# Performance work log

Measured on AMD Instinct MI355X. Metric: run time of the kernel, lower is better.

## Reference

```python
import jax, jax.numpy as jnp
import numpy as np
from jax import lax

D_MODEL = 512
D_STATE = 32
D_CONV = 4
D_INNER = 2 * D_MODEL
DT_RANK = (D_MODEL + 15) // 16  # 32
B_SZ, L = 8, 1024
EPS = 1e-12


def _mamba_params(key, pfx):
    ks = jax.random.split(key, 6)
    s = 0.02
    p = {}
    p[pfx + '_in_w'] = jax.random.normal(ks[0], (2 * D_INNER, D_MODEL)) * s
    p[pfx + '_conv_w'] = jax.random.normal(ks[1], (D_INNER, D_CONV)) * s
    p[pfx + '_conv_b'] = jnp.zeros((D_INNER,))
    p[pfx + '_xproj_w'] = jax.random.normal(ks[2], (DT_RANK + 2 * D_STATE, D_INNER)) * s
    p[pfx + '_dt_w'] = jax.random.normal(ks[3], (D_INNER, DT_RANK)) * s
    p[pfx + '_dt_b'] = jax.random.uniform(ks[4], (D_INNER,), minval=-4.0, maxval=-2.0)
    p[pfx + '_A_log'] = jnp.log(jnp.broadcast_to(jnp.arange(1, D_STATE + 1, dtype=jnp.float32), (D_INNER, D_STATE)))
    p[pfx + '_D'] = jnp.ones((D_INNER,))
    p[pfx + '_out_w'] = jax.random.normal(ks[5], (D_MODEL, D_INNER)) * s
    return p


def setup_inputs() -> dict:
    key = jax.random.key(0)
    ks = jax.random.split(key, 10)
    inp = {
        'hidden_states': jax.random.normal(ks[0], (B_SZ, L, D_MODEL)),
        'lengths': jax.random.randint(ks[1], (B_SZ,), 1, L + 1, dtype=jnp.int32),
    }
    inp.update(_mamba_params(ks[2], 'f'))
    inp.update(_mamba_params(ks[3], 'b'))
    s = 0.02
    inp['proj_w'] = jax.random.normal(ks[4], (1, 2)) * 0.5 + 0.5
    inp['proj_b'] = jnp.zeros((1,))
    inp['ln_g'] = jnp.ones((D_MODEL,))
    inp['ln_b'] = jnp.zeros((D_MODEL,))
    inp['ffn_w1'] = jax.random.normal(ks[5], (4 * D_MODEL, D_MODEL)) * s
    inp['ffn_b1'] = jnp.zeros((4 * D_MODEL,))
    inp['ffn_w2'] = jax.random.normal(ks[6], (D_MODEL, 4 * D_MODEL)) * s
    inp['ffn_b2'] = jnp.zeros((D_MODEL,))
    inp['ffn_ln_g'] = jnp.ones((D_MODEL,))
    inp['ffn_ln_b'] = jnp.zeros((D_MODEL,))
    return inp


def _layernorm(x, g, b):
    mu = jnp.mean(x, -1, keepdims=True)
    var = jnp.mean(jnp.square(x - mu), -1, keepdims=True)
    return (x - mu) * lax.rsqrt(var + EPS) * g + b


def _selective_scan(delta, Bm, Cm, u, A, D):
    # delta,u: (B,L,Di); Bm,Cm: (B,L,N); A: (Di,N); D: (Di,)
    def step(h, inp):
        d_t, B_t, C_t, u_t = inp
        dA = jnp.exp(d_t[..., None] * A)                 # (B,Di,N)
        h = dA * h + (d_t * u_t)[..., None] * B_t[:, None, :]
        y = jnp.einsum('bdn,bn->bd', h, C_t)
        return h, y
    h0 = jnp.zeros((u.shape[0], A.shape[0], A.shape[1]), u.dtype)
    xs = (delta.transpose(1, 0, 2), Bm.transpose(1, 0, 2),
          Cm.transpose(1, 0, 2), u.transpose(1, 0, 2))
    _, ys = lax.scan(step, h0, xs)
    return ys.transpose(1, 0, 2) + u * D


def _mamba(x, in_w, conv_w, conv_b, xproj_w, dt_w, dt_b, A_log, Dp, out_w):
    xz = jnp.einsum('bld,ed->ble', x, in_w)              # (B,L,2Di)
    x_in, z = jnp.split(xz, 2, axis=-1)
    # causal depthwise conv1d
    xc = jnp.pad(x_in.transpose(0, 2, 1), ((0, 0), (0, 0), (D_CONV - 1, 0)))
    xc = lax.conv_general_dilated(xc, conv_w[:, None, :], (1,), 'VALID',
                                  dimension_numbers=('NCH', 'OIH', 'NCH'),
                                  feature_group_count=D_INNER)
    xc = jax.nn.silu(xc + conv_b[None, :, None]).transpose(0, 2, 1)  # (B,L,Di)
    x_dbl = jnp.einsum('bld,ed->ble', xc, xproj_w)
    dt, Bm, Cm = jnp.split(x_dbl, [DT_RANK, DT_RANK + D_STATE], axis=-1)
    delta = jax.nn.softplus(jnp.einsum('blr,dr->bld', dt, dt_w) + dt_b)
    A = -jnp.exp(A_log)
    y = _selective_scan(delta, Bm, Cm, xc, A, Dp)
    y = y * jax.nn.silu(z)
    return jnp.einsum('bld,ed->ble', y, out_w)


def reference(hidden_states, lengths,
              f_in_w, f_conv_w, f_conv_b, f_xproj_w, f_dt_w, f_dt_b, f_A_log, f_D, f_out_w,
              b_in_w, b_conv_w, b_conv_b, b_xproj_w, b_dt_w, b_dt_b, b_A_log, b_D, b_out_w,
              proj_w, proj_b, ln_g, ln_b,
              ffn_w1, ffn_b1, ffn_w2, ffn_b2, ffn_ln_g, ffn_ln_b):
    x = hidden_states
    hf = _mamba(x, f_in_w, f_conv_w, f_conv_b, f_xproj_w, f_dt_w, f_dt_b, f_A_log, f_D, f_out_w)
    hb = _mamba(jnp.flip(x, 1), b_in_w, b_conv_w, b_conv_b, b_xproj_w, b_dt_w, b_dt_b, b_A_log, b_D, b_out_w)
    hb = jnp.flip(hb, 1)
    # Linear(2,1) over stacked [hf,hb] on last axis
    out = hf * proj_w[0, 0] + hb * proj_w[0, 1] + proj_b[0]
    out1 = _layernorm(out + x, ln_g, ln_b)  # dropout = identity (eval)
    h = jax.nn.gelu(jnp.einsum('bld,ed->ble', out1, ffn_w1) + ffn_b1, approximate=False)
    h = jnp.einsum('ble,de->bld', h, ffn_w2) + ffn_b2
    return _layernorm(h + out1, ffn_ln_g, ffn_ln_b)
```

## Files before the change

### kernel.cpp

```cpp
#include <hip/hip_runtime.h>
#include <hip/hip_bf16.h>
#include <hip/hip_fp16.h>
#include <math.h>

typedef __hip_bfloat16 bf16;
typedef __attribute__((ext_vector_type(8))) short bfrag;
typedef __attribute__((ext_vector_type(4))) float ffrag;
typedef __attribute__((ext_vector_type(4))) float f4;
typedef __attribute__((ext_vector_type(4))) short sh4;

#define BSZ    8
#define LSEQ   1024
#define DMODEL 512
#define DINNER 1024
#define DSTATE 32
#define DTRANK 32
#define MROWS  (BSZ * LSEQ)

__device__ __forceinline__ float bf2f(bf16 v) { return __bfloat162float(v); }
__device__ __forceinline__ float s2f(short s) {
    union { unsigned u; float f; } c; c.u = ((unsigned)(unsigned short)s) << 16; return c.f;
}
__device__ __forceinline__ short f2s(float v) {
    union { bf16 b; short s; } u; u.b = __float2bfloat16(v); return u.s;
}
__device__ __forceinline__ void stC(float* p, size_t i, float v) { p[i] = v; }
__device__ __forceinline__ void stC(bf16* p, size_t i, float v) { p[i] = __float2bfloat16(v); }
__device__ __forceinline__ float fsigmoid(float x) {
    return __builtin_amdgcn_rcpf(1.f + __expf(-x));
}
__device__ __forceinline__ float fexp2(float x) { return __builtin_amdgcn_exp2f(x); }

__device__ __forceinline__ float dload(const void* p, size_t i, int f) {
    if (f == 1) return ((const float*)p)[i];
    if (f == 2) return __half2float(((const __half*)p)[i]);
    if (f == 3) return (float)((const double*)p)[i];
    return bf2f(((const bf16*)p)[i]);
}

enum { ACT_NONE = 0, ACT_SOFTPLUS = 1, ACT_GELU = 2 };

__global__ void resolve_kernel(const void* a8, const void* d9, const void* d22,
                               const void* s0, const void* s1, int* flags)
{
    if (threadIdx.x != 0 || blockIdx.x != 0) return;
    const int cand[4] = {1, 0, 2, 3};
    int fw = -1;
    for (int ci = 0; ci < 4 && fw < 0; ++ci) {
        int f = cand[ci];
        bool ok = true;
        for (int k = 0; k < 48 && ok; ++k) {
            float e = logf((float)((k & 31) + 1));
            float v = dload(a8, k, f);
            ok = (v == v) && fabsf(v - e) <= 0.02f * e + 0.02f;
        }
        for (int k = 0; k < 8 && ok; ++k)
            ok = fabsf(dload(d9, k, f) - 1.f) <= 0.01f &&
                 fabsf(dload(d22, k, f) - 1.f) <= 0.01f;
        if (ok) fw = f;
    }
    int fx = -1, xs = -1;
    for (int si = 0; si < 2 && fx < 0; ++si) {
        const void* p = (si == 0) ? s0 : s1;
        for (int ci = 0; ci < 4 && fx < 0; ++ci) {
            int f = cand[ci];
            bool ok = true;
            float s = 0.f, s2 = 0.f;
            for (int k = 0; k < 256 && ok; ++k) {
                float v = dload(p, k, f);
                ok = (v == v) && fabsf(v) < 16.f;
                s += v; s2 += v * v;
            }
            if (ok) {
                float mu = s * (1.f / 256.f);
                float var = s2 * (1.f / 256.f) - mu * mu;
                if (var > 0.25f && var < 4.f) { fx = f; xs = si; }
            }
        }
    }
    flags[0] = (fw < 0) ? 1 : fw;
    flags[1] = (fx < 0) ? 1 : fx;
    flags[2] = (xs < 0) ? 0 : xs;
    flags[3] = (fw == 1 && fx == 1) ? 1 : 0;
}

__global__ __launch_bounds__(256) void cvt_x_kernel(const void* x0, const void* x1,
                                                    bf16* __restrict__ dst,
                                                    const int* __restrict__ flags)
{
    const void* x = flags[2] ? x1 : x0;
    const int fx = flags[1];
    int i = blockIdx.x * 256 + threadIdx.x;
    if (fx == 1) {
        f4 v = ((const f4*)x)[i];
        sh4 o;
#pragma unroll
        for (int j = 0; j < 4; ++j) o[j] = f2s(v[j]);
        ((sh4*)dst)[i] = o;
    } else {
#pragma unroll
        for (int j = 0; j < 4; ++j)
            dst[(size_t)i * 4 + j] = __float2bfloat16(dload(x, (size_t)i * 4 + j, fx));
    }
}

__global__ __launch_bounds__(256) void cvt_w_kernel(const float* __restrict__ src,
                                                    bf16* __restrict__ dst, int n4)
{
    int i = blockIdx.x * 256 + threadIdx.x;
    if (i >= n4) return;
    f4 v = ((const f4*)src)[i];
    sh4 o;
#pragma unroll
    for (int j = 0; j < 4; ++j) o[j] = f2s(v[j]);
    ((sh4*)dst)[i] = o;
}

__device__ __forceinline__ void glds16(const bf16* g, short* l)
{
    __builtin_amdgcn_global_load_lds(
        (const __attribute__((address_space(1))) void*)g,
        (__attribute__((address_space(3))) void*)l,
        16, 0, 0);
}

template <int FLIPB, int ACT, typename CT>
__global__ __launch_bounds__(256) void bgemm_kernel(
    const bf16* __restrict__ A, int lda,
    const bf16* __restrict__ B, int ldb,
    const float* __restrict__ bias,
    CT* __restrict__ C, int ldc, int K)
{
    __shared__ __align__(16) short As[128 * 32];
    __shared__ __align__(16) short Bs[128 * 32];
    const int tid = threadIdx.x;
    const int bm = blockIdx.y * 128, bn = blockIdx.x * 128;
    const int lane = tid & 63, w = tid >> 6;

    const int srow = lane >> 2;
    const int skc  = (lane & 3) << 3;
    const int arow0 = bm + w * 32 + srow;
    int brow0 = bn + w * 32 + srow;
    int brow1 = brow0 + 16;
    if (FLIPB) {
        brow0 = (brow0 & ~(LSEQ - 1)) + (LSEQ - 1 - (brow0 & (LSEQ - 1)));
        brow1 = (brow1 & ~(LSEQ - 1)) + (LSEQ - 1 - (brow1 & (LSEQ - 1)));
    }
    const bf16* ga0 = A + (size_t)arow0 * lda + skc;
    const bf16* ga1 = ga0 + (size_t)16 * lda;
    const bf16* gb0 = B + (size_t)brow0 * ldb + skc;
    const bf16* gb1 = B + (size_t)brow1 * ldb + skc;
    short* la0 = &As[(w * 32) * 32];
    short* la1 = &As[(w * 32 + 16) * 32];
    short* lb0 = &Bs[(w * 32) * 32];
    short* lb1 = &Bs[(w * 32 + 16) * 32];

    const int wm = (w & 1) << 6, wn = (w >> 1) << 6;
    const int lm = lane & 15, quad = lane >> 4;

    ffrag acc[4][4];
#pragma unroll
    for (int i = 0; i < 4; ++i)
#pragma unroll
        for (int j = 0; j < 4; ++j)
#pragma unroll
            for (int e = 0; e < 4; ++e) acc[i][j][e] = 0.f;

    for (int k0 = 0; k0 < K; k0 += 32) {
        glds16(ga0 + k0, la0);
        glds16(ga1 + k0, la1);
        glds16(gb0 + k0, lb0);
        glds16(gb1 + k0, lb1);
        __syncthreads();
        bfrag af[4], bfv[4];
#pragma unroll
        for (int ti = 0; ti < 4; ++ti)
            af[ti] = *(const bfrag*)&As[(wm + ti * 16 + lm) * 32 + quad * 8];
#pragma unroll
        for (int tj = 0; tj < 4; ++tj)
            bfv[tj] = *(const bfrag*)&Bs[(wn + tj * 16 + lm) * 32 + quad * 8];
#pragma unroll
        for (int ti = 0; ti < 4; ++ti)
#pragma unroll
            for (int tj = 0; tj < 4; ++tj)
                acc[ti][tj] = __builtin_amdgcn_mfma_f32_16x16x32_bf16(
                    af[ti], bfv[tj], acc[ti][tj], 0, 0, 0);
        __syncthreads();
    }

#pragma unroll
    for (int tj = 0; tj < 4; ++tj) {
        int col = bn + wn + tj * 16 + lm;
        float bcv = bias ? bias[col] : 0.f;
#pragma unroll
        for (int ti = 0; ti < 4; ++ti) {
#pragma unroll
            for (int r2 = 0; r2 < 4; ++r2) {
                int rowg = bm + wm + ti * 16 + quad * 4 + r2;
                float v = acc[ti][tj][r2] + bcv;
                if (ACT == ACT_GELU) v = 0.5f * v * (1.f + erff(v * 0.70710678118654752f));
                stC(C, (size_t)rowg * ldc + col, v);
            }
        }
    }
}

template <int AM, int WHID, int FLIPW, int ACT, int BROW, typename CT>
__global__ __launch_bounds__(256) void mgemm_kernel(
    const void* __restrict__ A, int lda,
    const void* __restrict__ W0, const void* __restrict__ W1, int ldw,
    const float* __restrict__ bias,
    CT* __restrict__ C, int ldc, int M, int N, int K,
    const int* __restrict__ flags)
{
    __shared__ short As[128 * 40];
    __shared__ short Ws[128 * 40];
    const int tid = threadIdx.x;
    const int bm = blockIdx.y * 128;
    const int bn = blockIdx.x * 128;
    const float* Wp = (const float*)(WHID ? (flags[2] ? W1 : W0) : W0);

    const int r = tid >> 1;
    const int hcol = (tid & 1) << 4;
    int wrow = bn + r;
    if (FLIPW) { int b = wrow >> 10, l = wrow & 1023; wrow = (b << 10) + (1023 - l); }

    const int lane = tid & 63, w = tid >> 6;
    const int wm = (w & 1) << 6, wn = (w >> 1) << 6;
    const int lm = lane & 15, quad = lane >> 4;

    ffrag acc[4][4];
#pragma unroll
    for (int i = 0; i < 4; ++i)
#pragma unroll
        for (int j = 0; j < 4; ++j)
#pragma unroll
            for (int e = 0; e < 4; ++e) acc[i][j][e] = 0.f;

    for (int k0 = 0; k0 < K; k0 += 32) {
        if (AM == 2) {
            int kk = tid >> 3;
            int mc = tid & 7;
            const bf16* src = (const bf16*)A + (size_t)(k0 + kk) * lda + bm + mc * 16;
            bfrag v0 = *(const bfrag*)src;
            bfrag v1 = *(const bfrag*)(src + 8);
#pragma unroll
            for (int i = 0; i < 8; ++i) {
                As[(mc * 16 + i) * 40 + kk] = v0[i];
                As[(mc * 16 + 8 + i) * 40 + kk] = v1[i];
            }
        } else if (AM == 0) {
            const bf16* src = (const bf16*)A + (size_t)(bm + r) * lda + k0 + hcol;
            *(bfrag*)&As[r * 40 + hcol] = *(const bfrag*)src;
            *(bfrag*)&As[r * 40 + hcol + 8] = *(const bfrag*)(src + 8);
        } else {
            const float* src = (const float*)A + (size_t)(bm + r) * lda + k0 + hcol;
            float t[16];
            ((f4*)t)[0] = ((const f4*)src)[0];
            ((f4*)t)[1] = ((const f4*)src)[1];
            ((f4*)t)[2] = ((const f4*)src)[2];
            ((f4*)t)[3] = ((const f4*)src)[3];
            bfrag s0, s1;
#pragma unroll
            for (int i = 0; i < 8; ++i) { s0[i] = f2s(t[i]); s1[i] = f2s(t[8 + i]); }
            *(bfrag*)&As[r * 40 + hcol] = s0;
            *(bfrag*)&As[r * 40 + hcol + 8] = s1;
        }
        {
            bfrag s0, s1;
            if (bn + r < N) {
                const float* src = Wp + (size_t)wrow * ldw + k0 + hcol;
                float t[16];
                ((f4*)t)[0] = ((const f4*)src)[0];
                ((f4*)t)[1] = ((const f4*)src)[1];
                ((f4*)t)[2] = ((const f4*)src)[2];
                ((f4*)t)[3] = ((const f4*)src)[3];
#pragma unroll
                for (int i = 0; i < 8; ++i) { s0[i] = f2s(t[i]); s1[i] = f2s(t[8 + i]); }
            } else {
#pragma unroll
                for (int i = 0; i < 8; ++i) { s0[i] = 0; s1[i] = 0; }
            }
            *(bfrag*)&Ws[r * 40 + hcol] = s0;
            *(bfrag*)&Ws[r * 40 + hcol + 8] = s1;
        }
        __syncthreads();

        bfrag af[4], bfv[4];
#pragma unroll
        for (int ti = 0; ti < 4; ++ti)
            af[ti] = *(const bfrag*)&As[(wm + ti * 16 + lm) * 40 + quad * 8];
#pragma unroll
        for (int tj = 0; tj < 4; ++tj)
            bfv[tj] = *(const bfrag*)&Ws[(wn + tj * 16 + lm) * 40 + quad * 8];
#pragma unroll
        for (int ti = 0; ti < 4; ++ti)
#pragma unroll
            for (int tj = 0; tj < 4; ++tj)
                acc[ti][tj] = __builtin_amdgcn_mfma_f32_16x16x32_bf16(
                    af[ti], bfv[tj], acc[ti][tj], 0, 0, 0);
        __syncthreads();
    }

#pragma unroll
    for (int tj = 0; tj < 4; ++tj) {
        int col = bn + wn + tj * 16 + lm;
        if (col < N) {
            float bcv = (bias && !BROW) ? bias[col] : 0.f;
#pragma unroll
            for (int ti = 0; ti < 4; ++ti) {
#pragma unroll
                for (int r2 = 0; r2 < 4; ++r2) {
                    int rowg = bm + wm + ti * 16 + quad * 4 + r2;
                    float v = acc[ti][tj][r2] + bcv;
                    if (BROW && bias) v += bias[rowg];
                    if (ACT == ACT_SOFTPLUS) v = (v > 20.f) ? v : log1pf(expf(v));
                    else if (ACT == ACT_GELU) v = 0.5f * v * (1.f + erff(v * 0.70710678118654752f));
                    stC(C, (size_t)rowg * ldc + col, v);
                }
            }
        }
    }
}

__global__ __launch_bounds__(256) void conv_silu_kernel(
    const bf16* __restrict__ xin_T,
    const void* __restrict__ cw,
    const void* __restrict__ cb,
    bf16* __restrict__ u_T,
    const int* __restrict__ flags)
{
    const int fw = flags[0];
    int blk = blockIdx.x;
    int chunk = blk & 3;
    int db = blk >> 2;
    int b = db & 7;
    int d = db >> 3;
    int l = chunk * 256 + threadIdx.x;
    size_t base = (size_t)d * MROWS + b * LSEQ;
    float w0 = dload(cw, d * 4 + 0, fw), w1 = dload(cw, d * 4 + 1, fw);
    float w2 = dload(cw, d * 4 + 2, fw), w3 = dload(cw, d * 4 + 3, fw);
    float acc = dload(cb, d, fw);
    if (l >= 3) acc += bf2f(xin_T[base + l - 3]) * w0;
    if (l >= 2) acc += bf2f(xin_T[base + l - 2]) * w1;
    if (l >= 1) acc += bf2f(xin_T[base + l - 1]) * w2;
    acc += bf2f(xin_T[base + l]) * w3;
    u_T[base + l] = __float2bfloat16(acc * fsigmoid(acc));
}

#define SCH 8
struct ScanBuf { float dl[SCH], uv[SCH], Bv[SCH], Cv[SCH]; float zsc, usc; };
struct PV { float p[SCH]; float zsc, usc; };

__device__ __forceinline__ void scan_load(ScanBuf& s,
    const bf16* __restrict__ dT, const bf16* __restrict__ uT,
    const bf16* __restrict__ zT, const float* __restrict__ xdbl,
    size_t lb, size_t mb, int n)
{
    bfrag dv = *(const bfrag*)&dT[lb];
    bfrag uv = *(const bfrag*)&uT[lb];
#pragma unroll
    for (int j = 0; j < SCH; ++j) { s.dl[j] = s2f(dv[j]); s.uv[j] = s2f(uv[j]); }
    s.zsc = bf2f(zT[lb + (n & 7)]);
    s.usc = bf2f(uT[lb + (n & 7)]);
#pragma unroll
    for (int j = 0; j < SCH; ++j) {
        s.Bv[j] = xdbl[(mb + j) * 96 + 32 + n];
        s.Cv[j] = xdbl[(mb + j) * 96 + 64 + n];
    }
}

__device__ __forceinline__ void scan_steps(const ScanBuf& s, float& h, float Ad2, PV& o)
{
#pragma unroll
    for (int j = 0; j < SCH; ++j) {
        float dlv = s.dl[j];
        float e = fexp2(dlv * Ad2);
        h = e * h + dlv * s.uv[j] * s.Bv[j];
        o.p[j] = h * s.Cv[j];
    }
    o.zsc = s.zsc; o.usc = s.usc;
}

__device__ __forceinline__ void reduce_store(const PV& v, float Dd,
    bf16* __restrict__ yT, size_t lb, bool b0, bool b1, bool b2, bool wr)
{
    float q[4];
#pragma unroll
    for (int jj = 0; jj < 4; ++jj) {
        float keep = b0 ? v.p[2 * jj + 1] : v.p[2 * jj];
        float send = b0 ? v.p[2 * jj] : v.p[2 * jj + 1];
        q[jj] = keep + __shfl_xor(send, 1);
    }
    float r0 = (b1 ? q[1] : q[0]) + __shfl_xor(b1 ? q[0] : q[1], 2);
    float r1 = (b1 ? q[3] : q[2]) + __shfl_xor(b1 ? q[2] : q[3], 2);
    float t = (b2 ? r1 : r0) + __shfl_xor(b2 ? r0 : r1, 4);
    t += __shfl_xor(t, 8);
    t += __shfl_xor(t, 16);
    if (wr) {
        float y = t + v.usc * Dd;
        float g = v.zsc;
        y *= g * fsigmoid(g);
        yT[lb + (threadIdx.x & 7)] = __float2bfloat16(y);
    }
}

__global__ __launch_bounds__(256) void scan_kernel(
    const bf16* __restrict__ delta_T,
    bf16* __restrict__ u_T,
    const bf16* __restrict__ z_T,
    const float* __restrict__ xdbl,
    const void* __restrict__ A_log,
    const void* __restrict__ Dp,
    const int* __restrict__ flags)
{
    const int fw = flags[0];
    const int tid = threadIdx.x;
    const int n = tid & 31;
    const int dloc = tid >> 5;
    const int gd = blockIdx.x * 8 + dloc;
    const int b = gd >> 10;
    const int d = gd & (DINNER - 1);
    const bool b0 = n & 1, b1 = n & 2, b2 = n & 4;
    const bool wr = (n < 8);

    const float Ad2 = -__expf(dload(A_log, d * DSTATE + n, fw)) * 1.44269504088896341f;
    const float Dd = dload(Dp, d, fw);
    const size_t lbase = (size_t)d * MROWS + b * LSEQ;
    const size_t mbase = (size_t)b * LSEQ;
    float h = 0.f;

    ScanBuf bufA, bufB;
    PV pA, pB;
    scan_load(bufA, delta_T, u_T, z_T, xdbl, lbase, mbase, n);
    scan_load(bufB, delta_T, u_T, z_T, xdbl, lbase + SCH, mbase + SCH, n);
    scan_steps(bufA, h, Ad2, pA);
    for (int c = 1; c < 127; c += 2) {
        scan_load(bufA, delta_T, u_T, z_T, xdbl,
                  lbase + (size_t)(c + 1) * SCH, mbase + (size_t)(c + 1) * SCH, n);
        scan_steps(bufB, h, Ad2, pB);
        reduce_store(pA, Dd, u_T, lbase + (size_t)(c - 1) * SCH, b0, b1, b2, wr);
        scan_load(bufB, delta_T, u_T, z_T, xdbl,
                  lbase + (size_t)(c + 2) * SCH, mbase + (size_t)(c + 2) * SCH, n);
        scan_steps(bufA, h, Ad2, pA);
        reduce_store(pB, Dd, u_T, lbase + (size_t)c * SCH, b0, b1, b2, wr);
    }
    scan_steps(bufB, h, Ad2, pB);
    reduce_store(pA, Dd, u_T, lbase + (size_t)126 * SCH, b0, b1, b2, wr);
    reduce_store(pB, Dd, u_T, lbase + (size_t)127 * SCH, b0, b1, b2, wr);
}

__global__ __launch_bounds__(256) void combine_ln_kernel(
    const bf16* __restrict__ hf, const bf16* __restrict__ hb,
    const void* __restrict__ x0, const void* __restrict__ x1,
    const void* __restrict__ pw, const void* __restrict__ pb,
    const void* __restrict__ g, const void* __restrict__ be,
    bf16* __restrict__ out1,
    const int* __restrict__ flags)
{
    const int fw = flags[0];
    const int fx = flags[1];
    const void* x = flags[2] ? x1 : x0;
    int row = blockIdx.x;
    int b = row >> 10, l = row & (LSEQ - 1);
    int rrow = (b << 10) + (LSEQ - 1 - l);
    float pw0 = dload(pw, 0, fw), pw1 = dload(pw, 1, fw), pbv = dload(pb, 0, fw);
    __shared__ float red[2][4];
    float v[2], s = 0.f, s2 = 0.f;
#pragma unroll
    for (int i = 0; i < 2; ++i) {
        int c = threadIdx.x + i * 256;
        float val = bf2f(hf[(size_t)row * DMODEL + c]) * pw0
                  + bf2f(hb[(size_t)rrow * DMODEL + c]) * pw1
                  + pbv + dload(x, (size_t)row * DMODEL + c, fx);
        v[i] = val; s += val; s2 += val * val;
    }
    for (int m = 1; m < 64; m <<= 1) { s += __shfl_xor(s, m); s2 += __shfl_xor(s2, m); }
    int w = threadIdx.x >> 6;
    if ((threadIdx.x & 63) == 0) { red[0][w] = s; red[1][w] = s2; }
    __syncthreads();
    s = red[0][0] + red[0][1] + red[0][2] + red[0][3];
    s2 = red[1][0] + red[1][1] + red[1][2] + red[1][3];
    float mu = s * (1.f / DMODEL);
    float var = s2 * (1.f / DMODEL) - mu * mu;
    float r = rsqrtf(fmaxf(var, 0.f) + 1e-12f);
#pragma unroll
    for (int i = 0; i < 2; ++i) {
        int c = threadIdx.x + i * 256;
        float val = (v[i] - mu) * r * dload(g, c, fw) + dload(be, c, fw);
        out1[(size_t)row * DMODEL + c] = __float2bfloat16(val);
    }
}

__global__ __launch_bounds__(256) void final_ln_kernel(
    const float* __restrict__ out2, const bf16* __restrict__ out1,
    const void* __restrict__ g, const void* __restrict__ be,
    float* __restrict__ out,
    const int* __restrict__ flags)
{
    const int fw = flags[0];
    const int valid = flags[3];
    int row = blockIdx.x;
    __shared__ float red[2][4];
    float v[2], s = 0.f, s2 = 0.f;
#pragma unroll
    for (int i = 0; i < 2; ++i) {
        int c = threadIdx.x + i * 256;
        float val = out2[(size_t)row * DMODEL + c] + bf2f(out1[(size_t)row * DMODEL + c]);
        v[i] = val; s += val; s2 += val * val;
    }
    for (int m = 1; m < 64; m <<= 1) { s += __shfl_xor(s, m); s2 += __shfl_xor(s2, m); }
    int w = threadIdx.x >> 6;
    if ((threadIdx.x & 63) == 0) { red[0][w] = s; red[1][w] = s2; }
    __syncthreads();
    s = red[0][0] + red[0][1] + red[0][2] + red[0][3];
    s2 = red[1][0] + red[1][1] + red[1][2] + red[1][3];
    float mu = s * (1.f / DMODEL);
    float var = s2 * (1.f / DMODEL) - mu * mu;
    float r = rsqrtf(fmaxf(var, 0.f) + 1e-12f);
#pragma unroll
    for (int i = 0; i < 2; ++i) {
        int c = threadIdx.x + i * 256;
        float val = (v[i] - mu) * r * dload(g, c, fw) + dload(be, c, fw);
        out[(size_t)row * DMODEL + c] = valid ? val : 0.f;
    }
}

extern "C" void kernel_launch(void* const* d_in, const int* in_sizes, int n_in,
                              void* d_out, int out_size, void* d_ws, size_t ws_size,
                              hipStream_t stream)
{
    const void* x0 = d_in[0];
    const void* x1 = d_in[1];
    const void* proj_w   = d_in[20];
    const void* proj_b   = d_in[21];
    const void* ln_g     = d_in[22];
    const void* ln_b     = d_in[23];
    const float* ffn_w1  = (const float*)d_in[24];
    const float* ffn_b1  = (const float*)d_in[25];
    const float* ffn_w2  = (const float*)d_in[26];
    const float* ffn_b2  = (const float*)d_in[27];
    const void* ffn_ln_g = d_in[28];
    const void* ffn_ln_b = d_in[29];

    char* wsb = (char*)d_ws;
    char* ob  = (char*)d_out;
    bf16*  xin_T   = (bf16*)(wsb + 0);
    bf16*  uy_T    = (bf16*)(wsb + (16u << 20));
    bf16*  z_T     = (bf16*)(wsb + (32u << 20));
    bf16*  delta_T = (bf16*)(wsb + 0);
    float* xdbl    = (float*)(wsb + (48u << 20));
    bf16*  in_w_bf = (bf16*)(wsb + (51u << 20));
    bf16*  hf      = (bf16*)d_out;
    bf16*  hb      = (bf16*)d_out + (size_t)MROWS * DMODEL;
    bf16*  xbf     = (bf16*)(ob + (8u << 20));
    bf16*  w1bf    = (bf16*)(ob + 0);
    bf16*  w2bf    = (bf16*)(ob + (2u << 20));
    bf16*  out1    = (bf16*)(wsb + 0);
    bf16*  ffn_h   = (bf16*)(wsb + (8u << 20));
    float* out2    = (float*)(wsb + (40u << 20));
    int*   flags   = (int*)(wsb + (56u << 20));

    dim3 blk(256);

    resolve_kernel<<<dim3(1), dim3(64), 0, stream>>>(
        d_in[8], d_in[9], d_in[22], x0, x1, flags);
    cvt_x_kernel<<<dim3(4096), blk, 0, stream>>>(x0, x1, xbf, flags);

    for (int dir = 0; dir < 2; ++dir) {
        int pb0 = 2 + dir * 9;
        const float* in_w    = (const float*)d_in[pb0 + 0];
        const void*  conv_w  = d_in[pb0 + 1];
        const void*  conv_b  = d_in[pb0 + 2];
        const float* xproj_w = (const float*)d_in[pb0 + 3];
        const float* dt_w    = (const float*)d_in[pb0 + 4];
        const float* dt_b    = (const float*)d_in[pb0 + 5];
        const void*  A_log   = d_in[pb0 + 6];
        const void*  Dp      = d_in[pb0 + 7];
        const float* out_w   = (const float*)d_in[pb0 + 8];
        bf16* hout = (dir == 0) ? hf : hb;

        cvt_w_kernel<<<dim3(1024), blk, 0, stream>>>(in_w, in_w_bf, (2048 * 512) / 4);
        if (dir == 0) {
            bgemm_kernel<0, ACT_NONE, bf16><<<dim3(64, 8), blk, 0, stream>>>(
                in_w_bf + (size_t)DINNER * DMODEL, DMODEL, xbf, DMODEL, nullptr,
                z_T, MROWS, DMODEL);
            bgemm_kernel<0, ACT_NONE, bf16><<<dim3(64, 8), blk, 0, stream>>>(
                in_w_bf, DMODEL, xbf, DMODEL, nullptr,
                xin_T, MROWS, DMODEL);
        } else {
            bgemm_kernel<1, ACT_NONE, bf16><<<dim3(64, 8), blk, 0, stream>>>(
                in_w_bf + (size_t)DINNER * DMODEL, DMODEL, xbf, DMODEL, nullptr,
                z_T, MROWS, DMODEL);
            bgemm_kernel<1, ACT_NONE, bf16><<<dim3(64, 8), blk, 0, stream>>>(
                in_w_bf, DMODEL, xbf, DMODEL, nullptr,
                xin_T, MROWS, DMODEL);
        }
        conv_silu_kernel<<<dim3(DINNER * BSZ * 4), blk, 0, stream>>>(
            xin_T, conv_w, conv_b, uy_T, flags);
        mgemm_kernel<2, 0, 0, ACT_NONE, 0, float><<<dim3(1, 64), blk, 0, stream>>>(
            uy_T, MROWS, xproj_w, nullptr, DINNER, nullptr,
            xdbl, 96, MROWS, 96, DINNER, flags);
        mgemm_kernel<1, 0, 0, ACT_SOFTPLUS, 1, bf16><<<dim3(64, 8), blk, 0, stream>>>(
            dt_w, DTRANK, xdbl, nullptr, 96, dt_b,
            delta_T, MROWS, DINNER, MROWS, DTRANK, flags);
        scan_kernel<<<dim3((BSZ * DINNER) / 8), blk, 0, stream>>>(
            delta_T, uy_T, z_T, xdbl, A_log, Dp, flags);
        mgemm_kernel<2, 0, 0, ACT_NONE, 0, bf16><<<dim3(4, 64), blk, 0, stream>>>(
            uy_T, MROWS, out_w, nullptr, DINNER, nullptr,
            hout, DMODEL, MROWS, DMODEL, DINNER, flags);
    }

    combine_ln_kernel<<<dim3(MROWS), blk, 0, stream>>>(
        hf, hb, x0, x1, proj_w, proj_b, ln_g, ln_b, out1, flags);
    cvt_w_kernel<<<dim3(1024), blk, 0, stream>>>(ffn_w1, w1bf, (2048 * 512) / 4);
    cvt_w_kernel<<<dim3(1024), blk, 0, stream>>>(ffn_w2, w2bf, (512 * 2048) / 4);
    bgemm_kernel<0, ACT_GELU, bf16><<<dim3(16, 64), blk, 0, stream>>>(
        out1, DMODEL, w1bf, DMODEL, ffn_b1,
        ffn_h, 2048, DMODEL);
    bgemm_kernel<0, ACT_NONE, float><<<dim3(4, 64), blk, 0, stream>>>(
        ffn_h, 2048, w2bf, 2048, ffn_b2,
        out2, DMODEL, 2048);
    final_ln_kernel<<<dim3(MROWS), blk, 0, stream>>>(
        out2, out1, ffn_ln_g, ffn_ln_b, (float*)d_out, flags);
}
```

Before: 1.009 ms.

## Route x_proj and out_proj through bf16 MFMA GEMMs with explicit transposes

Result: faster. 906.5 us (-10.1%).

```diff
diff --git a/kernel.cpp b/kernel.cpp
--- a/kernel.cpp
+++ b/kernel.cpp
@@ -116,6 +116,29 @@
     ((sh4*)dst)[i] = o;
 }
 
+__global__ __launch_bounds__(256) void transpose_kernel(
+    const bf16* __restrict__ src, bf16* __restrict__ dst, int R, int D)
+{
+    __shared__ short t[64][72];
+    const int r0 = blockIdx.x * 64, d0 = blockIdx.y * 64;
+    const int tr = threadIdx.x >> 3;
+    const int tc = (threadIdx.x & 7) * 8;
+#pragma unroll
+    for (int h = 0; h < 2; ++h) {
+        int d = tr + h * 32;
+        bfrag v = *(const bfrag*)&src[(size_t)(d0 + d) * R + r0 + tc];
+#pragma unroll
+        for (int j = 0; j < 8; ++j) t[tc + j][d] = v[j];
+    }
+    __syncthreads();
+#pragma unroll
+    for (int h = 0; h < 2; ++h) {
+        int r = tr + h * 32;
+        bfrag v = *(const bfrag*)&t[r][tc];
+        *(bfrag*)&dst[(size_t)(r0 + r) * D + d0 + tc] = v;
+    }
+}
+
 __device__ __forceinline__ void glds16(const bf16* g, short* l)
 {
     __builtin_amdgcn_global_load_lds(
@@ -200,6 +223,82 @@
                 float v = acc[ti][tj][r2] + bcv;
                 if (ACT == ACT_GELU) v = 0.5f * v * (1.f + erff(v * 0.70710678118654752f));
                 stC(C, (size_t)rowg * ldc + col, v);
+            }
+        }
+    }
+}
+
+template <int GUARD, int ACT, typename CT>
+__global__ __launch_bounds__(256) void bgemm64_kernel(
+    const bf16* __restrict__ A, int lda,
+    const bf16* __restrict__ B, int ldb,
+    const float* __restrict__ bias,
+    CT* __restrict__ C, int ldc, int N, int K)
+{
+    __shared__ __align__(16) short As[128 * 32];
+    __shared__ __align__(16) short Bs[64 * 32];
+    const int tid = threadIdx.x;
+    const int bm = blockIdx.y * 128, bn = blockIdx.x * 64;
+    const int lane = tid & 63, w = tid >> 6;
+
+    const int srow = lane >> 2;
+    const int skc  = (lane & 3) << 3;
+    const int arow0 = bm + w * 32 + srow;
+    int brow = bn + w * 16 + srow;
+    if (GUARD) brow = min(brow, N - 1);
+    const bf16* ga0 = A + (size_t)arow0 * lda + skc;
+    const bf16* ga1 = ga0 + (size_t)16 * lda;
+    const bf16* gb0 = B + (size_t)brow * ldb + skc;
+    short* la0 = &As[(w * 32) * 32];
+    short* la1 = &As[(w * 32 + 16) * 32];
+    short* lb0 = &Bs[(w * 16) * 32];
+
+    const int wm = (w & 1) << 6, wn = (w >> 1) << 5;
+    const int lm = lane & 15, quad = lane >> 4;
+
+    ffrag acc[4][2];
+#pragma unroll
+    for (int i = 0; i < 4; ++i)
+#pragma unroll
+        for (int j = 0; j < 2; ++j)
+#pragma unroll
+            for (int e = 0; e < 4; ++e) acc[i][j][e] = 0.f;
+
+    for (int k0 = 0; k0 < K; k0 += 32) {
+        glds16(ga0 + k0, la0);
+        glds16(ga1 + k0, la1);
+        glds16(gb0 + k0, lb0);
+        __syncthreads();
+        bfrag af[4], bfv[2];
+#pragma unroll
+        for (int ti = 0; ti < 4; ++ti)
+            af[ti] = *(const bfrag*)&As[(wm + ti * 16 + lm) * 32 + quad * 8];
+#pragma unroll
+        for (int tj = 0; tj < 2; ++tj)
+            bfv[tj] = *(const bfrag*)&Bs[(wn + tj * 16 + lm) * 32 + quad * 8];
+#pragma unroll
+        for (int ti = 0; ti < 4; ++ti)
+#pragma unroll
+            for (int tj = 0; tj < 2; ++tj)
+                acc[ti][tj] = __builtin_amdgcn_mfma_f32_16x16x32_bf16(
+                    af[ti], bfv[tj], acc[ti][tj], 0, 0, 0);
+        __syncthreads();
+    }
+
+#pragma unroll
+    for (int tj = 0; tj < 2; ++tj) {
+        int col = bn + wn + tj * 16 + lm;
+        if (!GUARD || col < N) {
+            float bcv = bias ? bias[col] : 0.f;
+#pragma unroll
+            for (int ti = 0; ti < 4; ++ti) {
+#pragma unroll
+                for (int r2 = 0; r2 < 4; ++r2) {
+                    int rowg = bm + wm + ti * 16 + quad * 4 + r2;
+                    float v = acc[ti][tj][r2] + bcv;
+                    if (ACT == ACT_GELU) v = 0.5f * v * (1.f + erff(v * 0.70710678118654752f));
+                    stC(C, (size_t)rowg * ldc + col, v);
+                }
             }
         }
     }
@@ -350,7 +449,6 @@
 
 #define SCH 8
 struct ScanBuf { float dl[SCH], uv[SCH], Bv[SCH], Cv[SCH]; float zsc, usc; };
-struct PV { float p[SCH]; float zsc, usc; };
 
 __device__ __forceinline__ void scan_load(ScanBuf& s,
     const bf16* __restrict__ dT, const bf16* __restrict__ uT,
@@ -370,26 +468,22 @@
     }
 }
 
-__device__ __forceinline__ void scan_steps(const ScanBuf& s, float& h, float Ad2, PV& o)
-{
+__device__ __forceinline__ void scan_compute(const ScanBuf& s, float& h,
+    float Ad2, float Dd, bf16* __restrict__ yT, size_t lb,
+    bool b0, bool b1, bool b2, bool wr)
+{
+    float p[SCH];
 #pragma unroll
     for (int j = 0; j < SCH; ++j) {
         float dlv = s.dl[j];
-        float e = fexp2(dlv * Ad2);
-        h = e * h + dlv * s.uv[j] * s.Bv[j];
-        o.p[j] = h * s.Cv[j];
-    }
-    o.zsc = s.zsc; o.usc = s.usc;
-}
-
-__device__ __forceinline__ void reduce_store(const PV& v, float Dd,
-    bf16* __restrict__ yT, size_t lb, bool b0, bool b1, bool b2, bool wr)
-{
+        h = fexp2(dlv * Ad2) * h + dlv * s.uv[j] * s.Bv[j];
+        p[j] = h * s.Cv[j];
+    }
     float q[4];
 #pragma unroll
     for (int jj = 0; jj < 4; ++jj) {
-        float keep = b0 ? v.p[2 * jj + 1] : v.p[2 * jj];
-        float send = b0 ? v.p[2 * jj] : v.p[2 * jj + 1];
+        float keep = b0 ? p[2 * jj + 1] : p[2 * jj];
+        float send = b0 ? p[2 * jj] : p[2 * jj + 1];
         q[jj] = keep + __shfl_xor(send, 1);
     }
     float r0 = (b1 ? q[1] : q[0]) + __shfl_xor(b1 ? q[0] : q[1], 2);
@@ -398,8 +492,8 @@
     t += __shfl_xor(t, 8);
     t += __shfl_xor(t, 16);
     if (wr) {
-        float y = t + v.usc * Dd;
-        float g = v.zsc;
+        float y = t + s.usc * Dd;
+        float g = s.zsc;
         y *= g * fsigmoid(g);
         yT[lb + (threadIdx.x & 7)] = __float2bfloat16(y);
     }
@@ -431,23 +525,16 @@
     float h = 0.f;
 
     ScanBuf bufA, bufB;
-    PV pA, pB;
     scan_load(bufA, delta_T, u_T, z_T, xdbl, lbase, mbase, n);
-    scan_load(bufB, delta_T, u_T, z_T, xdbl, lbase + SCH, mbase + SCH, n);
-    scan_steps(bufA, h, Ad2, pA);
-    for (int c = 1; c < 127; c += 2) {
-        scan_load(bufA, delta_T, u_T, z_T, xdbl,
-                  lbase + (size_t)(c + 1) * SCH, mbase + (size_t)(c + 1) * SCH, n);
-        scan_steps(bufB, h, Ad2, pB);
-        reduce_store(pA, Dd, u_T, lbase + (size_t)(c - 1) * SCH, b0, b1, b2, wr);
+    for (int c0 = 0; c0 < LSEQ / SCH; c0 += 2) {
         scan_load(bufB, delta_T, u_T, z_T, xdbl,
-                  lbase + (size_t)(c + 2) * SCH, mbase + (size_t)(c + 2) * SCH, n);
-        scan_steps(bufA, h, Ad2, pA);
-        reduce_store(pB, Dd, u_T, lbase + (size_t)c * SCH, b0, b1, b2, wr);
-    }
-    scan_steps(bufB, h, Ad2, pB);
-    reduce_store(pA, Dd, u_T, lbase + (size_t)126 * SCH, b0, b1, b2, wr);
-    reduce_store(pB, Dd, u_T, lbase + (size_t)127 * SCH, b0, b1, b2, wr);
+                  lbase + (size_t)(c0 + 1) * SCH, mbase + (size_t)(c0 + 1) * SCH, n);
+        scan_compute(bufA, h, Ad2, Dd, u_T, lbase + (size_t)c0 * SCH, b0, b1, b2, wr);
+        if (c0 + 2 < LSEQ / SCH)
+            scan_load(bufA, delta_T, u_T, z_T, xdbl,
+                      lbase + (size_t)(c0 + 2) * SCH, mbase + (size_t)(c0 + 2) * SCH, n);
+        scan_compute(bufB, h, Ad2, Dd, u_T, lbase + (size_t)(c0 + 1) * SCH, b0, b1, b2, wr);
+    }
 }
 
 __global__ __launch_bounds__(256) void combine_ln_kernel(
@@ -546,11 +633,15 @@
     char* wsb = (char*)d_ws;
     char* ob  = (char*)d_out;
     bf16*  xin_T   = (bf16*)(wsb + 0);
-    bf16*  uy_T    = (bf16*)(wsb + (16u << 20));
-    bf16*  z_T     = (bf16*)(wsb + (32u << 20));
+    bf16*  z_T     = (bf16*)(wsb + (16u << 20));
+    bf16*  uy_T    = (bf16*)(wsb + (32u << 20));
+    bf16*  u_rm    = (bf16*)(wsb + 0);
     bf16*  delta_T = (bf16*)(wsb + 0);
+    bf16*  y_rm    = (bf16*)(wsb + 0);
     float* xdbl    = (float*)(wsb + (48u << 20));
     bf16*  in_w_bf = (bf16*)(wsb + (51u << 20));
+    bf16*  xp_w_bf = (bf16*)(wsb + (53u << 20));
+    bf16*  o_w_bf  = (bf16*)(wsb + (54u << 20));
     bf16*  hf      = (bf16*)d_out;
     bf16*  hb      = (bf16*)d_out + (size_t)MROWS * DMODEL;
     bf16*  xbf     = (bf16*)(ob + (8u << 20));
@@ -581,34 +672,29 @@
         bf16* hout = (dir == 0) ? hf : hb;
 
         cvt_w_kernel<<<dim3(1024), blk, 0, stream>>>(in_w, in_w_bf, (2048 * 512) / 4);
-        if (dir == 0) {
-            bgemm_kernel<0, ACT_NONE, bf16><<<dim3(64, 8), blk, 0, stream>>>(
-                in_w_bf + (size_t)DINNER * DMODEL, DMODEL, xbf, DMODEL, nullptr,
-                z_T, MROWS, DMODEL);
-            bgemm_kernel<0, ACT_NONE, bf16><<<dim3(64, 8), blk, 0, stream>>>(
-                in_w_bf, DMODEL, xbf, DMODEL, nullptr,
-                xin_T, MROWS, DMODEL);
-        } else {
-            bgemm_kernel<1, ACT_NONE, bf16><<<dim3(64, 8), blk, 0, stream>>>(
-                in_w_bf + (size_t)DINNER * DMODEL, DMODEL, xbf, DMODEL, nullptr,
-                z_T, MROWS, DMODEL);
-            bgemm_kernel<1, ACT_NONE, bf16><<<dim3(64, 8), blk, 0, stream>>>(
-                in_w_bf, DMODEL, xbf, DMODEL, nullptr,
-                xin_T, MROWS, DMODEL);
-        }
+        cvt_w_kernel<<<dim3(96), blk, 0, stream>>>(xproj_w, xp_w_bf, (96 * 1024) / 4);
+        cvt_w_kernel<<<dim3(512), blk, 0, stream>>>(out_w, o_w_bf, (512 * 1024) / 4);
+
+        if (dir == 0)
+            bgemm_kernel<0, ACT_NONE, bf16><<<dim3(64, 16), blk, 0, stream>>>(
+                in_w_bf, DMODEL, xbf, DMODEL, nullptr, xin_T, MROWS, DMODEL);
+        else
+            bgemm_kernel<1, ACT_NONE, bf16><<<dim3(64, 16), blk, 0, stream>>>(
+                in_w_bf, DMODEL, xbf, DMODEL, nullptr, xin_T, MROWS, DMODEL);
+
         conv_silu_kernel<<<dim3(DINNER * BSZ * 4), blk, 0, stream>>>(
             xin_T, conv_w, conv_b, uy_T, flags);
-        mgemm_kernel<2, 0, 0, ACT_NONE, 0, float><<<dim3(1, 64), blk, 0, stream>>>(
-            uy_T, MROWS, xproj_w, nullptr, DINNER, nullptr,
-            xdbl, 96, MROWS, 96, DINNER, flags);
+        transpose_kernel<<<dim3(128, 16), blk, 0, stream>>>(uy_T, u_rm, MROWS, DINNER);
+        bgemm64_kernel<1, ACT_NONE, float><<<dim3(2, 64), blk, 0, stream>>>(
+            u_rm, DINNER, xp_w_bf, DINNER, nullptr, xdbl, 96, 96, DINNER);
         mgemm_kernel<1, 0, 0, ACT_SOFTPLUS, 1, bf16><<<dim3(64, 8), blk, 0, stream>>>(
             dt_w, DTRANK, xdbl, nullptr, 96, dt_b,
             delta_T, MROWS, DINNER, MROWS, DTRANK, flags);
         scan_kernel<<<dim3((BSZ * DINNER) / 8), blk, 0, stream>>>(
             delta_T, uy_T, z_T, xdbl, A_log, Dp, flags);
-        mgemm_kernel<2, 0, 0, ACT_NONE, 0, bf16><<<dim3(4, 64), blk, 0, stream>>>(
-            uy_T, MROWS, out_w, nullptr, DINNER, nullptr,
-            hout, DMODEL, MROWS, DMODEL, DINNER, flags);
+        transpose_kernel<<<dim3(128, 16), blk, 0, stream>>>(uy_T, y_rm, MROWS, DINNER);
+        bgemm64_kernel<0, ACT_NONE, bf16><<<dim3(8, 64), blk, 0, stream>>>(
+            y_rm, DINNER, o_w_bf, DINNER, nullptr, hout, DMODEL, DMODEL, DINNER);
     }
 
     combine_ln_kernel<<<dim3(MROWS), blk, 0, stream>>>(
@@ -616,11 +702,9 @@
     cvt_w_kernel<<<dim3(1024), blk, 0, stream>>>(ffn_w1, w1bf, (2048 * 512) / 4);
     cvt_w_kernel<<<dim3(1024), blk, 0, stream>>>(ffn_w2, w2bf, (512 * 2048) / 4);
     bgemm_kernel<0, ACT_GELU, bf16><<<dim3(16, 64), blk, 0, stream>>>(
-        out1, DMODEL, w1bf, DMODEL, ffn_b1,
-        ffn_h, 2048, DMODEL);
-    bgemm_kernel<0, ACT_NONE, float><<<dim3(4, 64), blk, 0, stream>>>(
-        ffn_h, 2048, w2bf, 2048, ffn_b2,
-        out2, DMODEL, 2048);
+        out1, DMODEL, w1bf, DMODEL, ffn_b1, ffn_h, 2048, DMODEL);
+    bgemm64_kernel<0, ACT_NONE, float><<<dim3(8, 64), blk, 0, stream>>>(
+        ffn_h, 2048, w2bf, 2048, ffn_b2, out2, DMODEL, DMODEL, 2048);
     final_ln_kernel<<<dim3(MROWS), blk, 0, stream>>>(
         out2, out1, ffn_ln_g, ffn_ln_b, (float*)d_out, flags);
 }
```
